# Optimization experiments

Hardware: AMD Instinct MI355X
Metric: run time of the kernel (lower is better)

## Reference

```python
import jax, jax.numpy as jnp
import numpy as np

B = 1024
P = 8
D = 2048
NUM_IDS = 64
MARGIN = 0.3
EPS = 1e-12


def setup_inputs() -> dict:
    key = jax.random.key(0)
    k1, k2, k3 = jax.random.split(key, 3)
    feats = jax.random.normal(k1, (B, P * D), dtype=jnp.float32)
    labels = jax.random.randint(k2, (B,), 0, NUM_IDS, dtype=jnp.int64)
    subs = jax.random.randint(k3, (B,), 0, 2, dtype=jnp.int64)
    return {"feats": feats, "labels": labels, "subs": subs}


def reference(feats, labels, subs):
    b = feats.shape[0]
    f = feats.reshape(b, -1, D)  # [B, P, D]
    dt = f.dtype

    # Per-sample class centers via a single segment-mean pass
    # (equivalent to the original per-sample boolean-mask mean loop).
    seg_sum = jax.ops.segment_sum(f, labels, num_segments=NUM_IDS)  # [NUM_IDS, P, D]
    counts = jax.ops.segment_sum(jnp.ones((b,), dt), labels, num_segments=NUM_IDS)
    centers_by_id = seg_sum / jnp.maximum(counts, 1.0)[:, None, None]
    centers = centers_by_id[labels]  # [B, P, D]

    # dist_ap[i] = sum_p ||f[i,p] - center[i,p]||
    d_ap = jnp.sqrt(jnp.clip(jnp.sum((f - centers) ** 2, axis=-1), EPS, None)).sum(-1)  # [B]
    dist_ap = d_ap[:, None] + d_ap[None, :]  # [B, B]

    # pairwise_distance: dist_aa[i,j] = sum_p ||f[i,p] - f[j,p]||, via gemm trick
    sq = jnp.sum(f * f, axis=-1)  # [B, P]
    inner = jnp.einsum('ipd,jpd->ijp', f, f)  # [B, B, P]
    d2 = sq[:, None, :] + sq[None, :, :] - 2.0 * inner
    dist_aa = jnp.sqrt(jnp.clip(d2, EPS, None)).sum(-1)  # [B, B]

    # masked margin loss over negative (different-label) pairs
    mask = labels[:, None] != labels[None, :]  # [B, B] bool
    vals = jnp.clip(dist_ap - dist_aa + MARGIN, 0.0, None)
    maskf = mask.astype(dt)
    loss = jnp.sum(vals * maskf) / jnp.sum(maskf)
    return loss
```

## Files before the change

### kernel.cpp

```cpp
#include <hip/hip_runtime.h>
#include <hip/hip_bf16.h>

#define B_ 1024
#define P_ 8
#define D_ 2048
#define FD_ (P_ * D_)
#define NID 64
#define MARGIN_ 0.3f
#define EPS_ 1e-12f

typedef unsigned short u16;
typedef float float4_t __attribute__((ext_vector_type(4)));

__device__ __forceinline__ float bf2f(unsigned v) {
    unsigned x = v << 16;
    float f;
    __builtin_memcpy(&f, &x, 4);
    return f;
}

static const size_t OFF_COUNTS = 0;
static const size_t OFF_OFFS   = 256;
static const size_t OFF_PERM   = 512;
static const size_t OFF_NEG    = 4608;
static const size_t OFF_POS    = 8168;
static const size_t OFF_TICKET = 8172;
static const size_t OFF_S      = 8192;
static const size_t OFF_SQ     = 40960;
static const size_t OFF_DAP    = 73728;
static const size_t OFF_FB     = 131072;
static const size_t OFF_PD     = OFF_FB + (size_t)B_ * FD_;


__global__ void k_prep(const float* __restrict__ feats, const int* __restrict__ labels,
                       unsigned char* __restrict__ fb, float* __restrict__ sq,
                       float* countsf, int* offs, int* perm, float* negcnt) {
    int tid = threadIdx.x;
    __shared__ __align__(16) unsigned char st[32768];
    if (blockIdx.x < 512) {
        const int p = blockIdx.x & 7;
        const int rb = blockIdx.x >> 3;
        const int r = tid >> 4;
        const int s = tid & 15;
        const int i = rb * 16 + r;
        const float* frow = feats + (size_t)i * FD_ + p * D_;
        const int ks_lo = (s >> 1);
        const int lhi0 = (s & 1) * 2;
        float s2 = 0.f;
#pragma unroll
        for (int it = 0; it < 8; it++) {
            int d = it * 256 + s * 16;
            float4 f0 = *(const float4*)(frow + d);
            float4 f1 = *(const float4*)(frow + d + 4);
            float4 f2 = *(const float4*)(frow + d + 8);
            float4 f3 = *(const float4*)(frow + d + 12);
            s2 += f0.x*f0.x + f0.y*f0.y + f0.z*f0.z + f0.w*f0.w
                + f1.x*f1.x + f1.y*f1.y + f1.z*f1.z + f1.w*f1.w
                + f2.x*f2.x + f2.y*f2.y + f2.z*f2.z + f2.w*f2.w
                + f3.x*f3.x + f3.y*f3.y + f3.z*f3.z + f3.w*f3.w;
            unsigned u0 = (unsigned)__builtin_amdgcn_cvt_pk_fp8_f32(f0.x, f0.y, 0, false);
            u0 = (unsigned)__builtin_amdgcn_cvt_pk_fp8_f32(f0.z, f0.w, (int)u0, true);
            unsigned u1 = (unsigned)__builtin_amdgcn_cvt_pk_fp8_f32(f1.x, f1.y, 0, false);
            u1 = (unsigned)__builtin_amdgcn_cvt_pk_fp8_f32(f1.z, f1.w, (int)u1, true);
            unsigned u2 = (unsigned)__builtin_amdgcn_cvt_pk_fp8_f32(f2.x, f2.y, 0, false);
            u2 = (unsigned)__builtin_amdgcn_cvt_pk_fp8_f32(f2.z, f2.w, (int)u2, true);
            unsigned u3 = (unsigned)__builtin_amdgcn_cvt_pk_fp8_f32(f3.x, f3.y, 0, false);
            u3 = (unsigned)__builtin_amdgcn_cvt_pk_fp8_f32(f3.z, f3.w, (int)u3, true);
            int ks = it * 8 + ks_lo;
            *(uint2*)&st[ks * 512 + lhi0 * 128 + r * 8] = make_uint2(u0, u1);
            *(uint2*)&st[ks * 512 + (lhi0 + 1) * 128 + r * 8] = make_uint2(u2, u3);
        }
        s2 += __shfl_xor(s2, 1, 64);
        s2 += __shfl_xor(s2, 2, 64);
        s2 += __shfl_xor(s2, 4, 64);
        s2 += __shfl_xor(s2, 8, 64);
        if (s == 0) sq[i * 8 + p] = s2;
        __syncthreads();
        unsigned char* dst = fb + (size_t)p * 2097152 + (size_t)rb * 32768;
#pragma unroll
        for (int c = 0; c < 8; c++) {
            int off = tid * 128 + c * 16;
            *(uint4*)(dst + off) = *(const uint4*)&st[off];
        }
    } else {
        __shared__ int h[NID], o[NID], cur[NID];
        if (tid < NID) h[tid] = 0;
        __syncthreads();
        for (int i = tid; i < B_; i += 256) atomicAdd(&h[labels[i]], 1);
        __syncthreads();
        if (tid == 0) {
            int acc = 0;
            long long ss = 0;
            for (int c = 0; c < NID; c++) {
                o[c] = acc;
                acc += h[c];
                ss += (long long)h[c] * h[c];
            }
            *negcnt = (float)((long long)B_ * B_ - ss);
        }
        __syncthreads();
        if (tid < NID) {
            countsf[tid] = (float)h[tid];
            offs[tid] = o[tid];
            cur[tid] = o[tid];
        }
        __syncthreads();
        for (int i = tid; i < B_; i += 256) {
            int pos = atomicAdd(&cur[labels[i]], 1);
            perm[pos] = i;
        }
    }
}

__global__ __launch_bounds__(128) void k_pairs(const unsigned char* __restrict__ fb,
                                               const float* __restrict__ sq,
                                               const int* __restrict__ labels,
                                               float* __restrict__ S,
                                               u16* __restrict__ pd) {
    const int p = blockIdx.x;
    int rem = blockIdx.y, tu = 0;
    while (rem >= 16 - tu) { rem -= 16 - tu; tu++; }
    const int tv = tu + rem;
    const int i0 = tu * 64, j0 = tv * 64;

    __shared__ __align__(16) float ep[4096];
    __shared__ float sqAs[64], sqBs[64];
    __shared__ int labA[64], labB[64];
    const int tid = threadIdx.x;
    const int lane = tid & 63;
    const int h = tid >> 6;
    if (tid < 64) {
        sqAs[tid] = sq[(i0 + tid) * 8 + p];
        labA[tid] = labels[i0 + tid];
    } else {
        sqBs[lane] = sq[(j0 + lane) * 8 + p];
        labB[lane] = labels[j0 + lane];
    }

    const unsigned char* base = fb + (size_t)p * 2097152 + (size_t)lane * 8;
    const unsigned char* pA[4];
    const unsigned char* pB[4];
#pragma unroll
    for (int a = 0; a < 4; a++) {
        pA[a] = base + (size_t)(tu * 4 + a) * 32768 + (size_t)h * 32 * 512;
        pB[a] = base + (size_t)(tv * 4 + a) * 32768 + (size_t)h * 32 * 512;
    }

    float4_t acc[4][4];
#pragma unroll
    for (int a = 0; a < 4; a++)
#pragma unroll
        for (int b = 0; b < 4; b++) acc[a][b] = (float4_t){0.f, 0.f, 0.f, 0.f};

#pragma unroll 4
    for (int t = 0; t < 32; t++) {
        const int koff = t * 512;
        long af[4], bf[4];
#pragma unroll
        for (int a = 0; a < 4; a++) {
            af[a] = *(const long*)(pA[a] + koff);
            bf[a] = *(const long*)(pB[a] + koff);
        }
#pragma unroll
        for (int a = 0; a < 4; a++)
#pragma unroll
            for (int b = 0; b < 4; b++)
                acc[a][b] = __builtin_amdgcn_mfma_f32_16x16x32_fp8_fp8(
                    af[a], bf[b], acc[a][b], 0, 0, 0);
    }

    if (h == 1) {
#pragma unroll
        for (int a = 0; a < 4; a++)
#pragma unroll
            for (int b = 0; b < 4; b++)
                *(float4_t*)&ep[((a * 4 + b) * 64 + lane) * 4] = acc[a][b];
    }
    __syncthreads();
    if (h == 0) {
        const int lhi = lane >> 4, llo = lane & 15;
        u16* outp = pd + (size_t)p * B_ * B_;
        float rs[4][4];
        float cs[4];
#pragma unroll
        for (int a = 0; a < 4; a++)
#pragma unroll
            for (int r = 0; r < 4; r++) rs[a][r] = 0.f;
#pragma unroll
        for (int b = 0; b < 4; b++) cs[b] = 0.f;
#pragma unroll
        for (int a = 0; a < 4; a++) {
            int la0 = labA[a * 16 + lhi * 4 + 0];
            int la1 = labA[a * 16 + lhi * 4 + 1];
            int la2 = labA[a * 16 + lhi * 4 + 2];
            int la3 = labA[a * 16 + lhi * 4 + 3];
#pragma unroll
            for (int b = 0; b < 4; b++) {
                float4_t o = *(const float4_t*)&ep[((a * 4 + b) * 64 + lane) * 4];
                int jl = b * 16 + llo;
                int lb = labB[jl];
#pragma unroll
                for (int r = 0; r < 4; r++) {
                    int il = a * 16 + lhi * 4 + r;
                    float t = acc[a][b][r] + o[r];
                    float d2 = sqAs[il] + sqBs[jl] - 2.0f * t;
                    outp[(size_t)(i0 + il) * B_ + (j0 + jl)] =
                        __bfloat16_as_ushort(__float2bfloat16(sqrtf(fmaxf(d2, EPS_))));
                    int la = (r == 0) ? la0 : (r == 1) ? la1 : (r == 2) ? la2 : la3;
                    if (lb == la) {
                        rs[a][r] += t;
                        cs[b] += t;
                    }
                }
            }
        }
#pragma unroll
        for (int a = 0; a < 4; a++)
#pragma unroll
            for (int r = 0; r < 4; r++) {
                float v = rs[a][r];
                v += __shfl_xor(v, 1, 64);
                v += __shfl_xor(v, 2, 64);
                v += __shfl_xor(v, 4, 64);
                v += __shfl_xor(v, 8, 64);
                if (llo == 0)
                    atomicAdd(&S[(size_t)(i0 + a * 16 + lhi * 4 + r) * 8 + p], v);
            }
        if (tv > tu) {
#pragma unroll
            for (int b = 0; b < 4; b++) {
                float v = cs[b];
                v += __shfl_xor(v, 16, 64);
                v += __shfl_xor(v, 32, 64);
                if (lhi == 0)
                    atomicAdd(&S[(size_t)(j0 + b * 16 + llo) * 8 + p], v);
            }
        }
    }
}

__global__ void k_dap(const float* __restrict__ S, const float* __restrict__ sq,
                      const float* __restrict__ countsf, const int* __restrict__ offs,
                      const int* __restrict__ perm, float* __restrict__ dap) {
    int c = blockIdx.x;
    int tid = threadIdx.x;
    int cnt = (int)countsf[c];
    int off = offs[c];
    __shared__ float T[8];
    if (tid < 8) {
        float t = 0.f;
        for (int m = 0; m < cnt; m++) t += S[(size_t)perm[off + m] * 8 + tid];
        T[tid] = t;
    }
    __syncthreads();
    float n = fmaxf((float)cnt, 1.f);
    float inv = 1.f / n, inv2 = inv * inv;
    for (int m = tid; m < cnt; m += 64) {
        int i = perm[off + m];
        float d = 0.f;
#pragma unroll
        for (int p = 0; p < 8; p++) {
            float d2 = sq[i * 8 + p] - 2.f * inv * S[(size_t)i * 8 + p] + inv2 * T[p];
            d += sqrtf(fmaxf(d2, EPS_));
        }
        dap[i] = d;
    }
}

__global__ void k_lossred(const u16* __restrict__ pd, const float* __restrict__ dap,
                          const int* __restrict__ labels, float* possum,
                          const float* negcnt, int* ticket, float* out) {
    int i = blockIdx.x;
    int tid = threadIdx.x;
    float di = dap[i];
    int li = labels[i];
    float lsum = 0.f;
    for (int j = i + 1 + tid; j < B_; j += 256) {
        if (labels[j] != li) {
            float daa = 0.f;
#pragma unroll
            for (int p = 0; p < 8; p++)
                daa += bf2f(pd[((size_t)p << 20) + (size_t)i * B_ + j]);
            lsum += fmaxf(di + dap[j] - daa + MARGIN_, 0.f);
        }
    }
    lsum *= 2.0f;
    for (int o = 32; o; o >>= 1) lsum += __shfl_down(lsum, o, 64);
    __shared__ float red[4];
    int wid = tid >> 6, lane = tid & 63;
    if (lane == 0) red[wid] = lsum;
    __syncthreads();
    if (tid == 0) {
        atomicAdd(possum, red[0] + red[1] + red[2] + red[3]);
        __threadfence();
        int t = atomicAdd(ticket, 1);
        if (t == B_ - 1) {
            float total = atomicAdd(possum, 0.0f);
            out[0] = total / negcnt[0];
        }
    }
}

extern "C" void kernel_launch(void* const* d_in, const int* in_sizes, int n_in,
                              void* d_out, int out_size, void* d_ws, size_t ws_size,
                              hipStream_t stream) {
    const float* feats = (const float*)d_in[0];
    const int* labels  = (const int*)d_in[1];
    float* out = (float*)d_out;

    char* w = (char*)d_ws;
    float* countsf = (float*)(w + OFF_COUNTS);
    int* offs      = (int*)(w + OFF_OFFS);
    int* perm      = (int*)(w + OFF_PERM);
    float* negcnt  = (float*)(w + OFF_NEG);
    float* possum  = (float*)(w + OFF_POS);
    int* ticket    = (int*)(w + OFF_TICKET);
    float* S       = (float*)(w + OFF_S);
    float* sq      = (float*)(w + OFF_SQ);
    float* dap     = (float*)(w + OFF_DAP);
    unsigned char* fb = (unsigned char*)(w + OFF_FB);
    u16* pd        = (u16*)(w + OFF_PD);

    hipMemsetAsync(w + OFF_POS, 0, (OFF_S - OFF_POS) + (size_t)B_ * P_ * 4, stream);

    k_prep<<<513, 256, 0, stream>>>(feats, labels, fb, sq, countsf, offs, perm, negcnt);
    k_pairs<<<dim3(8, 136), 128, 0, stream>>>(fb, sq, labels, S, pd);
    k_dap<<<NID, 64, 0, stream>>>(S, sq, countsf, offs, perm, dap);
    k_lossred<<<B_, 256, 0, stream>>>(pd, dap, labels, possum, negcnt, ticket, out);
}
```

Baseline: 196.3 us.

## Split K across four waves in pair kernel and fuse dap into last block

The pair GEMM kernel now runs 256 threads, so four waves each cover a quarter of the K range instead of two halves. Their partial results are combined through two LDS buffers in a two-stage reduction. The separate dap kernel is removed: the last k_pairs block to finish, found with an atomic ticket, computes the per-class center distances. The host memset is replaced by zeroing inside k_prep's histogram block. This cuts two launches and adds parallelism per tile, at the cost of extra LDS, more barriers and a serial tail in the final block.

Result: slower. 219.3 us (+11.7%).

```diff
diff --git a/kernel.cpp b/kernel.cpp
--- a/kernel.cpp
+++ b/kernel.cpp
@@ -8,6 +8,7 @@
 #define NID 64
 #define MARGIN_ 0.3f
 #define EPS_ 1e-12f
+#define NPAIRBLK (8 * 136)
 
 typedef unsigned short u16;
 typedef float float4_t __attribute__((ext_vector_type(4)));
@@ -19,22 +20,24 @@
     return f;
 }
 
-static const size_t OFF_COUNTS = 0;
-static const size_t OFF_OFFS   = 256;
-static const size_t OFF_PERM   = 512;
-static const size_t OFF_NEG    = 4608;
-static const size_t OFF_POS    = 8168;
-static const size_t OFF_TICKET = 8172;
-static const size_t OFF_S      = 8192;
-static const size_t OFF_SQ     = 40960;
-static const size_t OFF_DAP    = 73728;
-static const size_t OFF_FB     = 131072;
-static const size_t OFF_PD     = OFF_FB + (size_t)B_ * FD_;
+static const size_t OFF_COUNTS  = 0;
+static const size_t OFF_OFFS    = 256;
+static const size_t OFF_PERM    = 512;
+static const size_t OFF_NEG     = 4608;
+static const size_t OFF_POS     = 8160;
+static const size_t OFF_TICKET  = 8164;
+static const size_t OFF_TICKET2 = 8168;
+static const size_t OFF_S       = 8192;
+static const size_t OFF_SQ      = 40960;
+static const size_t OFF_DAP     = 73728;
+static const size_t OFF_FB      = 131072;
+static const size_t OFF_PD      = OFF_FB + (size_t)B_ * FD_;
 
 
 __global__ void k_prep(const float* __restrict__ feats, const int* __restrict__ labels,
                        unsigned char* __restrict__ fb, float* __restrict__ sq,
-                       float* countsf, int* offs, int* perm, float* negcnt) {
+                       float* countsf, int* offs, int* perm, float* negcnt,
+                       float* zbase ) {
     int tid = threadIdx.x;
     __shared__ __align__(16) unsigned char st[32768];
     if (blockIdx.x < 512) {
@@ -83,6 +86,7 @@
             *(uint4*)(dst + off) = *(const uint4*)&st[off];
         }
     } else {
+        for (int k = tid; k < 8 + 1024 * 8; k += 256) zbase[k] = 0.f;
         __shared__ int h[NID], o[NID], cur[NID];
         if (tid < NID) h[tid] = 0;
         __syncthreads();
@@ -112,38 +116,46 @@
     }
 }
 
-__global__ __launch_bounds__(128) void k_pairs(const unsigned char* __restrict__ fb,
-                                               const float* __restrict__ sq,
-                                               const int* __restrict__ labels,
-                                               float* __restrict__ S,
-                                               u16* __restrict__ pd) {
+__global__ __launch_bounds__(256, 4) void k_pairs(const unsigned char* __restrict__ fb,
+                                                  const float* __restrict__ sq,
+                                                  const int* __restrict__ labels,
+                                                  float* __restrict__ S,
+                                                  u16* __restrict__ pd,
+                                                  const float* __restrict__ countsf,
+                                                  const int* __restrict__ offs,
+                                                  const int* __restrict__ perm,
+                                                  float* __restrict__ dap,
+                                                  int* ticket2) {
     const int p = blockIdx.x;
     int rem = blockIdx.y, tu = 0;
     while (rem >= 16 - tu) { rem -= 16 - tu; tu++; }
     const int tv = tu + rem;
     const int i0 = tu * 64, j0 = tv * 64;
 
-    __shared__ __align__(16) float ep[4096];
+    __shared__ __align__(16) float cb0[4096];
+    __shared__ __align__(16) float cb1[4096];
     __shared__ float sqAs[64], sqBs[64];
     __shared__ int labA[64], labB[64];
+    __shared__ int lastflag;
     const int tid = threadIdx.x;
     const int lane = tid & 63;
     const int h = tid >> 6;
     if (tid < 64) {
         sqAs[tid] = sq[(i0 + tid) * 8 + p];
         labA[tid] = labels[i0 + tid];
-    } else {
+    } else if (tid < 128) {
         sqBs[lane] = sq[(j0 + lane) * 8 + p];
         labB[lane] = labels[j0 + lane];
     }
 
-    const unsigned char* base = fb + (size_t)p * 2097152 + (size_t)lane * 8;
+    const unsigned char* base = fb + (size_t)p * 2097152 + (size_t)lane * 8
+                              + (size_t)h * 16 * 512;
     const unsigned char* pA[4];
     const unsigned char* pB[4];
 #pragma unroll
     for (int a = 0; a < 4; a++) {
-        pA[a] = base + (size_t)(tu * 4 + a) * 32768 + (size_t)h * 32 * 512;
-        pB[a] = base + (size_t)(tv * 4 + a) * 32768 + (size_t)h * 32 * 512;
+        pA[a] = base + (size_t)(tu * 4 + a) * 32768;
+        pB[a] = base + (size_t)(tv * 4 + a) * 32768;
     }
 
     float4_t acc[4][4];
@@ -152,8 +164,8 @@
 #pragma unroll
         for (int b = 0; b < 4; b++) acc[a][b] = (float4_t){0.f, 0.f, 0.f, 0.f};
 
-#pragma unroll 4
-    for (int t = 0; t < 32; t++) {
+#pragma unroll 2
+    for (int t = 0; t < 16; t++) {
         const int koff = t * 512;
         long af[4], bf[4];
 #pragma unroll
@@ -174,7 +186,35 @@
         for (int a = 0; a < 4; a++)
 #pragma unroll
             for (int b = 0; b < 4; b++)
-                *(float4_t*)&ep[((a * 4 + b) * 64 + lane) * 4] = acc[a][b];
+                *(float4_t*)&cb0[((a * 4 + b) * 64 + lane) * 4] = acc[a][b];
+    } else if (h == 3) {
+#pragma unroll
+        for (int a = 0; a < 4; a++)
+#pragma unroll
+            for (int b = 0; b < 4; b++)
+                *(float4_t*)&cb1[((a * 4 + b) * 64 + lane) * 4] = acc[a][b];
+    }
+    __syncthreads();
+    if (h == 0) {
+#pragma unroll
+        for (int a = 0; a < 4; a++)
+#pragma unroll
+            for (int b = 0; b < 4; b++)
+                acc[a][b] += *(const float4_t*)&cb0[((a * 4 + b) * 64 + lane) * 4];
+    } else if (h == 2) {
+#pragma unroll
+        for (int a = 0; a < 4; a++)
+#pragma unroll
+            for (int b = 0; b < 4; b++)
+                acc[a][b] += *(const float4_t*)&cb1[((a * 4 + b) * 64 + lane) * 4];
+    }
+    __syncthreads();
+    if (h == 2) {
+#pragma unroll
+        for (int a = 0; a < 4; a++)
+#pragma unroll
+            for (int b = 0; b < 4; b++)
+                *(float4_t*)&cb0[((a * 4 + b) * 64 + lane) * 4] = acc[a][b];
     }
     __syncthreads();
     if (h == 0) {
@@ -196,7 +236,7 @@
             int la3 = labA[a * 16 + lhi * 4 + 3];
 #pragma unroll
             for (int b = 0; b < 4; b++) {
-                float4_t o = *(const float4_t*)&ep[((a * 4 + b) * 64 + lane) * 4];
+                float4_t o = *(const float4_t*)&cb0[((a * 4 + b) * 64 + lane) * 4];
                 int jl = b * 16 + llo;
                 int lb = labB[jl];
 #pragma unroll
@@ -237,33 +277,40 @@
             }
         }
     }
-}
-
-__global__ void k_dap(const float* __restrict__ S, const float* __restrict__ sq,
-                      const float* __restrict__ countsf, const int* __restrict__ offs,
-                      const int* __restrict__ perm, float* __restrict__ dap) {
-    int c = blockIdx.x;
-    int tid = threadIdx.x;
-    int cnt = (int)countsf[c];
-    int off = offs[c];
-    __shared__ float T[8];
-    if (tid < 8) {
-        float t = 0.f;
-        for (int m = 0; m < cnt; m++) t += S[(size_t)perm[off + m] * 8 + tid];
-        T[tid] = t;
-    }
-    __syncthreads();
-    float n = fmaxf((float)cnt, 1.f);
-    float inv = 1.f / n, inv2 = inv * inv;
-    for (int m = tid; m < cnt; m += 64) {
-        int i = perm[off + m];
-        float d = 0.f;
-#pragma unroll
-        for (int p = 0; p < 8; p++) {
-            float d2 = sq[i * 8 + p] - 2.f * inv * S[(size_t)i * 8 + p] + inv2 * T[p];
-            d += sqrtf(fmaxf(d2, EPS_));
-        }
-        dap[i] = d;
+    if (tid == 0) {
+        __threadfence();
+        int t = atomicAdd(ticket2, 1);
+        lastflag = (t == NPAIRBLK - 1) ? 1 : 0;
+    }
+    __syncthreads();
+    if (lastflag) {
+        __threadfence();
+        if (tid < NID) {
+            int c = tid;
+            int cnt = (int)countsf[c];
+            int off = offs[c];
+            float T[8];
+#pragma unroll
+            for (int q = 0; q < 8; q++) T[q] = 0.f;
+            for (int m = 0; m < cnt; m++) {
+                int i = perm[off + m];
+#pragma unroll
+                for (int q = 0; q < 8; q++) T[q] += S[(size_t)i * 8 + q];
+            }
+            float n = fmaxf((float)cnt, 1.f);
+            float inv = 1.f / n, inv2 = inv * inv;
+            for (int m = 0; m < cnt; m++) {
+                int i = perm[off + m];
+                float d = 0.f;
+#pragma unroll
+                for (int q = 0; q < 8; q++) {
+                    float d2 = sq[i * 8 + q] - 2.f * inv * S[(size_t)i * 8 + q]
+                             + inv2 * T[q];
+                    d += sqrtf(fmaxf(d2, EPS_));
+                }
+                dap[i] = d;
+            }
+        }
     }
 }
 
@@ -315,16 +362,16 @@
     float* negcnt  = (float*)(w + OFF_NEG);
     float* possum  = (float*)(w + OFF_POS);
     int* ticket    = (int*)(w + OFF_TICKET);
+    int* ticket2   = (int*)(w + OFF_TICKET2);
     float* S       = (float*)(w + OFF_S);
     float* sq      = (float*)(w + OFF_SQ);
     float* dap     = (float*)(w + OFF_DAP);
     unsigned char* fb = (unsigned char*)(w + OFF_FB);
     u16* pd        = (u16*)(w + OFF_PD);
 
-    hipMemsetAsync(w + OFF_POS, 0, (OFF_S - OFF_POS) + (size_t)B_ * P_ * 4, stream);
-
-    k_prep<<<513, 256, 0, stream>>>(feats, labels, fb, sq, countsf, offs, perm, negcnt);
-    k_pairs<<<dim3(8, 136), 128, 0, stream>>>(fb, sq, labels, S, pd);
-    k_dap<<<NID, 64, 0, stream>>>(S, sq, countsf, offs, perm, dap);
+    k_prep<<<513, 256, 0, stream>>>(feats, labels, fb, sq, countsf, offs, perm, negcnt,
+                                    (float*)(w + OFF_POS));
+    k_pairs<<<dim3(8, 136), 256, 0, stream>>>(fb, sq, labels, S, pd,
+                                              countsf, offs, perm, dap, ticket2);
     k_lossred<<<B_, 256, 0, stream>>>(pd, dap, labels, possum, negcnt, ticket, out);
 }
```
